# Performance work log

Measured on AMD Instinct MI355X. Metric: run time of the kernel, lower is better.

Reference implementation:

```python
import jax, jax.numpy as jnp
import numpy as np

K = 16  # num_samples (kNN neighbors)


def setup_inputs() -> dict:
    key = jax.random.key(0)
    k1, k2, k3 = jax.random.split(key, 3)
    B, N, S, D = 8, 8192, 2048, 64
    return {
        "points": jax.random.normal(k1, (B, 3, N), dtype=jnp.float32),
        "new_points": jax.random.normal(k2, (B, 3, S), dtype=jnp.float32),
        "features": jax.random.normal(k3, (B, D, N), dtype=jnp.float32),
    }


def reference(points, new_points, features):
    # channel-first -> channel-last, matching torch permute(0,2,1)
    pts = jnp.transpose(points, (0, 2, 1))       # [B, N, 3]
    newp = jnp.transpose(new_points, (0, 2, 1))  # [B, S, 3]
    feat = jnp.transpose(features, (0, 2, 1))    # [B, N, D]
    B, S, C = newp.shape

    # square_distance(points, new_points): [B, N, S]
    d = (
        jnp.sum(pts * pts, axis=-1)[:, :, None]
        - 2.0 * jnp.einsum("bnc,bsc->bns", pts, newp)
        + jnp.sum(newp * newp, axis=-1)[:, None, :]
    )
    # k smallest over N per (b, s): torch topk(largest=False) along dim=1 then permute -> [B, S, K]
    _, ind = jax.lax.top_k(-jnp.transpose(d, (0, 2, 1)), K)  # [B, S, K]

    gather = jax.vmap(lambda a, i: a[i])  # per-batch fancy gather
    grouped_pts = gather(pts, ind)    # [B, S, K, 3]
    grouped_feat = gather(feat, ind)  # [B, S, K, D]

    grouped_pts_new = grouped_pts - newp[:, :, None, :]          # relative coords
    new_features = jnp.concatenate([grouped_pts_new, grouped_feat], axis=-1)  # [B, S, K, 3+D]
    return jnp.transpose(new_features, (0, 3, 2, 1))  # [B, 3+D, K, S]
```

## Files before the change

### kernel.cpp

```cpp
#include <hip/hip_runtime.h>

constexpr int B = 8, N = 8192, S = 2048, D = 64, K = 16, C = 3 + D;
constexpr int G = 4;

__device__ __forceinline__ unsigned sortable(float f) {
    unsigned u = __float_as_uint(f);
    unsigned mask = (unsigned)(((int)u) >> 31) | 0x80000000u;
    return u ^ mask;
}

__device__ __forceinline__ float uload(const float* p) {
    return __uint_as_float(__builtin_amdgcn_readfirstlane(__float_as_uint(*p)));
}

__device__ __forceinline__ float make_d(float px, float py, float pz, float pnv,
                                        float qx, float qy, float qz, float qn) {
    float dot = __fmaf_rn(pz, qz, __fmaf_rn(py, qy, __fmul_rn(px, qx)));
    return __fadd_rn(__fsub_rn(pnv, __fmul_rn(2.0f, dot)), qn);
}

__device__ __forceinline__ float make_v(float px, float py, float pz, float pnv,
                                        float q2x, float q2y, float q2z) {
    float dot2 = __fmaf_rn(pz, q2z, __fmaf_rn(py, q2y, __fmul_rn(px, q2x)));
    return __fsub_rn(pnv, dot2);
}

__device__ __forceinline__ float bitonic_sort64_f32(float v, int lane) {
#pragma unroll
    for (int k = 2; k <= 64; k <<= 1)
#pragma unroll
        for (int j = k >> 1; j > 0; j >>= 1) {
            float o = __shfl_xor(v, j, 64);
            bool keepmin = ((lane & k) == 0) == ((lane & j) == 0);
            float mn = fminf(v, o), mx = fmaxf(v, o);
            v = keepmin ? mn : mx;
        }
    return v;
}

__device__ __forceinline__ unsigned long long bitonic_sort64_u64(unsigned long long v, int lane) {
#pragma unroll
    for (int k = 2; k <= 64; k <<= 1)
#pragma unroll
        for (int j = k >> 1; j > 0; j >>= 1) {
            unsigned long long o = __shfl_xor(v, j, 64);
            bool keepmin = ((lane & k) == 0) == ((lane & j) == 0);
            v = ((v < o) == keepmin) ? v : o;
        }
    return v;
}

__global__ void pack_kernel(const float* __restrict__ pts, float4* __restrict__ pts4) {
    int t = blockIdx.x * blockDim.x + threadIdx.x;
    if (t >= B * N) return;
    int b = t >> 13, n = t & (N - 1);
    const float* P = pts + (size_t)b * 3 * N;
    float x = P[n], y = P[N + n], z = P[2 * N + n];
    float pn = __fadd_rn(__fadd_rn(__fmul_rn(z, z), __fmul_rn(y, y)), __fmul_rn(x, x));
    pts4[t] = make_float4(x, y, z, pn);
}

__global__ void __launch_bounds__(256) transpose_kernel(const float* __restrict__ feat,
                                                        float* __restrict__ featT) {
    __shared__ float tile[64][65];
    int b = blockIdx.x >> 7;
    int n0 = (blockIdx.x & 127) << 6;
    int col = threadIdx.x & 63;
    int crow = threadIdx.x >> 6;
    const float* F = feat + (size_t)b * D * N;
#pragma unroll
    for (int i = 0; i < 16; ++i) {
        int c = i * 4 + crow;
        tile[c][col] = F[(size_t)c * N + n0 + col];
    }
    __syncthreads();
    float* FT = featT + ((size_t)b * N + n0) * D;
#pragma unroll
    for (int i = 0; i < 16; ++i) {
        int nl = i * 4 + crow;
        FT[(size_t)nl * D + col] = tile[col][nl];
    }
}

__global__ void __launch_bounds__(256) knn_kernel(const float4* __restrict__ pts4,
                                                  const float* __restrict__ newp,
                                                  int* __restrict__ ind) {
    __shared__ unsigned long long buf[4][G][64];
    __shared__ int cnt_lds[4][G];
    int wib = threadIdx.x >> 6;
    int lane = threadIdx.x & 63;
    int wid = blockIdx.x * 4 + wib;
    int b = wid >> 9;
    int sbase = (wid & 511) * G;
    const float4* P4 = pts4 + (size_t)b * N;
    const float* Q = newp + (size_t)b * 3 * S;
    if (lane < G) cnt_lds[wib][lane] = 0;
    float qx[G], qy[G], qz[G], qn[G], q2x[G], q2y[G], q2z[G];
#pragma unroll
    for (int g = 0; g < G; ++g) {
        int s = sbase + g;
        qx[g] = uload(Q + s);
        qy[g] = uload(Q + S + s);
        qz[g] = uload(Q + 2 * S + s);
        qn[g] = __fadd_rn(__fadd_rn(__fmul_rn(qz[g], qz[g]), __fmul_rn(qy[g], qy[g])),
                          __fmul_rn(qx[g], qx[g]));
        q2x[g] = 2.0f * qx[g];
        q2y[g] = 2.0f * qy[g];
        q2z[g] = 2.0f * qz[g];
    }

    float m[G];
#pragma unroll
    for (int g = 0; g < G; ++g) m[g] = __int_as_float(0x7f800000);
    for (int blk = 0; blk < N / 256; ++blk) {
        int nb = blk * 256 + lane;
        float4 c0 = P4[nb], c1 = P4[nb + 64], c2 = P4[nb + 128], c3 = P4[nb + 192];
#pragma unroll
        for (int g = 0; g < G; ++g) {
            float v0 = make_v(c0.x, c0.y, c0.z, c0.w, q2x[g], q2y[g], q2z[g]);
            float v1 = make_v(c1.x, c1.y, c1.z, c1.w, q2x[g], q2y[g], q2z[g]);
            float v2 = make_v(c2.x, c2.y, c2.z, c2.w, q2x[g], q2y[g], q2z[g]);
            float v3 = make_v(c3.x, c3.y, c3.z, c3.w, q2x[g], q2y[g], q2z[g]);
            m[g] = fminf(m[g], fminf(fminf(v0, v1), fminf(v2, v3)));
        }
    }
    float tau_d[G], vthr[G];
#pragma unroll
    for (int g = 0; g < G; ++g) {
        float tau_v = __shfl(bitonic_sort64_f32(m[g], lane), 15, 64);
        tau_d[g] = __fadd_rn(tau_v, qn[g]);
        vthr[g] = __fadd_rn(__fsub_rn(tau_d[g], qn[g]), 1e-4f);
    }

    for (int blk = 0; blk < N / 256; ++blk) {
        int nb = blk * 256 + lane;
        float4 c0 = P4[nb], c1 = P4[nb + 64], c2 = P4[nb + 128], c3 = P4[nb + 192];
#pragma unroll
        for (int g = 0; g < G; ++g) {
            float vv[4];
            vv[0] = make_v(c0.x, c0.y, c0.z, c0.w, q2x[g], q2y[g], q2z[g]);
            vv[1] = make_v(c1.x, c1.y, c1.z, c1.w, q2x[g], q2y[g], q2z[g]);
            vv[2] = make_v(c2.x, c2.y, c2.z, c2.w, q2x[g], q2y[g], q2z[g]);
            vv[3] = make_v(c3.x, c3.y, c3.z, c3.w, q2x[g], q2y[g], q2z[g]);
#pragma unroll
            for (int i = 0; i < 4; ++i) {
                if (vv[i] <= vthr[g]) {
                    float d = __fadd_rn(vv[i], qn[g]);
                    if (d <= tau_d[g]) {
                        int pos = atomicAdd(&cnt_lds[wib][g], 1);
                        if (pos < 64)
                            buf[wib][g][pos] =
                                ((unsigned long long)sortable(d) << 32) | (unsigned)(nb + i * 64);
                    }
                }
            }
        }
    }
    __syncthreads();

#pragma unroll
    for (int g = 0; g < G; ++g) {
        int cnt = cnt_lds[wib][g];
        int* my_ind = ind + ((size_t)b * S + sbase + g) * K;
        if (cnt <= 64) {
            unsigned long long key = (lane < cnt) ? buf[wib][g][lane] : ~0ull;
            key = bitonic_sort64_u64(key, lane);
            if (lane < K) my_ind[lane] = (int)(unsigned)key;
        } else {
            unsigned long long a[K];
#pragma unroll
            for (int i = 0; i < K; ++i) a[i] = ~0ull;
            for (int n = lane; n < N; n += 64) {
                float4 c = P4[n];
                float d = make_d(c.x, c.y, c.z, c.w, qx[g], qy[g], qz[g], qn[g]);
                unsigned long long key = ((unsigned long long)sortable(d) << 32) | (unsigned)n;
                if (key < a[K - 1]) {
#pragma unroll
                    for (int i = K - 1; i >= 1; --i) {
                        unsigned long long lo = a[i - 1];
                        a[i] = key < lo ? lo : (key < a[i] ? key : a[i]);
                    }
                    a[0] = key < a[0] ? key : a[0];
                }
            }
            for (int r = 0; r < K; ++r) {
                unsigned long long best = a[0];
#pragma unroll
                for (int mm = 1; mm < 64; mm <<= 1) {
                    unsigned long long o = __shfl_xor(best, mm, 64);
                    best = o < best ? o : best;
                }
                if (lane == 0) my_ind[r] = (int)(unsigned)best;
                bool won = (a[0] == best);
#pragma unroll
                for (int i = 0; i < K - 1; ++i) a[i] = won ? a[i + 1] : a[i];
                a[K - 1] = won ? ~0ull : a[K - 1];
            }
        }
    }
}

__global__ void __launch_bounds__(256) gather_tile_kernel(const float4* __restrict__ pts4,
                                                          const float* __restrict__ newp,
                                                          const float* __restrict__ featT,
                                                          const int* __restrict__ ind,
                                                          float* __restrict__ out) {
    __shared__ float tile[64][69];
    int bid = blockIdx.x;
    int b = bid >> 9;
    int k = (bid >> 5) & (K - 1);
    int s0 = (bid & 31) << 6;
    int j = threadIdx.x >> 2;
    int p = threadIdx.x & 3;
    int s = s0 + j;
    int id = ind[((size_t)b * S + s) * K + k];
    const float* row = featT + ((size_t)b * N + id) * D;
#pragma unroll
    for (int i = 0; i < 4; ++i) {
        int f = p + 4 * i;
        float4 v = *(const float4*)(row + f * 4);
        *(float4*)(&tile[j][3 + f * 4]) = v;
    }
    if (p == 0) {
        float4 pt = pts4[(size_t)b * N + id];
        const float* Q = newp + (size_t)b * 3 * S;
        tile[j][0] = __fsub_rn(pt.x, Q[s]);
        tile[j][1] = __fsub_rn(pt.y, Q[S + s]);
        tile[j][2] = __fsub_rn(pt.z, Q[2 * S + s]);
    }
    __syncthreads();
    size_t KS = (size_t)K * S;
    float* ob = out + ((size_t)b * C * K + k) * S + s0;
#pragma unroll
    for (int it = 0; it < 17; ++it) {
        int c = it * 4 + (threadIdx.x >> 6);
        int l = threadIdx.x & 63;
        if (c < C) ob[(size_t)c * KS + l] = tile[l][c];
    }
}

__global__ void __launch_bounds__(256) gather_kernel(const float4* __restrict__ pts4,
                                                     const float* __restrict__ newp,
                                                     const float* __restrict__ feat,
                                                     const int* __restrict__ ind,
                                                     float* __restrict__ out) {
    int t = blockIdx.x * blockDim.x + threadIdx.x;
    int s = t & (S - 1);
    int k = (t >> 11) & (K - 1);
    int rest = t >> 15;
    int g = rest % 17;
    int b = rest / 17;
    if (b >= B) return;
    int id = ind[((size_t)b * S + s) * K + k];
    size_t KS = (size_t)K * S;
    if (g == 0) {
        float4 p = pts4[(size_t)b * N + id];
        const float* Q = newp + (size_t)b * 3 * S;
        float* o = out + ((size_t)b * C * K + k) * S + s;
        o[0] = __fsub_rn(p.x, Q[s]);
        o[KS] = __fsub_rn(p.y, Q[S + s]);
        o[2 * KS] = __fsub_rn(p.z, Q[2 * S + s]);
    } else {
        int cb = (g - 1) * 4;
        const float* F = feat + (size_t)b * D * N;
        float4 f = make_float4(F[(size_t)cb * N + id], F[(size_t)(cb + 1) * N + id],
                               F[(size_t)(cb + 2) * N + id], F[(size_t)(cb + 3) * N + id]);
        float* o = out + (((size_t)b * C + 3 + cb) * K + k) * S + s;
        o[0] = f.x;
        o[KS] = f.y;
        o[2 * KS] = f.z;
        o[3 * KS] = f.w;
    }
}

extern "C" void kernel_launch(void* const* d_in, const int* in_sizes, int n_in,
                              void* d_out, int out_size, void* d_ws, size_t ws_size,
                              hipStream_t stream) {
    const float* pts = (const float*)d_in[0];
    const float* newp = (const float*)d_in[1];
    const float* feat = (const float*)d_in[2];
    float* out = (float*)d_out;

    size_t off_ind = 0;
    size_t off_pts4 = (size_t)B * S * K * sizeof(int);
    size_t off_featT = off_pts4 + (size_t)B * N * sizeof(float4);
    size_t need = off_featT + (size_t)B * N * D * sizeof(float);
    int* ind = (int*)((char*)d_ws + off_ind);
    float4* pts4 = (float4*)((char*)d_ws + off_pts4);
    float* featT = (float*)((char*)d_ws + off_featT);
    int useT = (ws_size >= need) ? 1 : 0;

    pack_kernel<<<(B * N) / 256, 256, 0, stream>>>(pts, pts4);
    if (useT) transpose_kernel<<<B * (N / 64), 256, 0, stream>>>(feat, featT);
    knn_kernel<<<(B * S) / (G * 4), 256, 0, stream>>>(pts4, newp, ind);
    if (useT)
        gather_tile_kernel<<<B * K * (S / 64), 256, 0, stream>>>(pts4, newp, featT, ind, out);
    else
        gather_kernel<<<(B * 17 * K * S) / 256, 256, 0, stream>>>(pts4, newp, feat, ind, out);
}
```

Baseline: 91.79 us.

## Estimate kNN threshold from a point subset and enlarge candidate buffer

The first pass, which estimates the 16th-nearest distance threshold, now scans only the first 2048 points instead of all 8192. That cuts the cost of this pass by three quarters. The looser threshold admits more candidates, so the per-query LDS buffer grows from 64 to 192 entries. The final bitonic sort is replaced by 16 rounds of wave-wide min extraction over three registers per lane. The risks are more atomics and LDS use in the second pass and more overflow into the slow full-scan fallback.

```diff
diff --git a/kernel.cpp b/kernel.cpp
--- a/kernel.cpp
+++ b/kernel.cpp
@@ -2,6 +2,8 @@
 
 constexpr int B = 8, N = 8192, S = 2048, D = 64, K = 16, C = 3 + D;
 constexpr int G = 4;
+constexpr int M = 2048;
+constexpr int BUFD = 192;
 
 __device__ __forceinline__ unsigned sortable(float f) {
     unsigned u = __float_as_uint(f);
@@ -34,18 +36,6 @@
             bool keepmin = ((lane & k) == 0) == ((lane & j) == 0);
             float mn = fminf(v, o), mx = fmaxf(v, o);
             v = keepmin ? mn : mx;
-        }
-    return v;
-}
-
-__device__ __forceinline__ unsigned long long bitonic_sort64_u64(unsigned long long v, int lane) {
-#pragma unroll
-    for (int k = 2; k <= 64; k <<= 1)
-#pragma unroll
-        for (int j = k >> 1; j > 0; j >>= 1) {
-            unsigned long long o = __shfl_xor(v, j, 64);
-            bool keepmin = ((lane & k) == 0) == ((lane & j) == 0);
-            v = ((v < o) == keepmin) ? v : o;
         }
     return v;
 }
@@ -85,7 +75,7 @@
 __global__ void __launch_bounds__(256) knn_kernel(const float4* __restrict__ pts4,
                                                   const float* __restrict__ newp,
                                                   int* __restrict__ ind) {
-    __shared__ unsigned long long buf[4][G][64];
+    __shared__ unsigned long long buf[4][G][BUFD];
     __shared__ int cnt_lds[4][G];
     int wib = threadIdx.x >> 6;
     int lane = threadIdx.x & 63;
@@ -95,24 +85,21 @@
     const float4* P4 = pts4 + (size_t)b * N;
     const float* Q = newp + (size_t)b * 3 * S;
     if (lane < G) cnt_lds[wib][lane] = 0;
-    float qx[G], qy[G], qz[G], qn[G], q2x[G], q2y[G], q2z[G];
+    float qn[G], q2x[G], q2y[G], q2z[G];
 #pragma unroll
     for (int g = 0; g < G; ++g) {
         int s = sbase + g;
-        qx[g] = uload(Q + s);
-        qy[g] = uload(Q + S + s);
-        qz[g] = uload(Q + 2 * S + s);
-        qn[g] = __fadd_rn(__fadd_rn(__fmul_rn(qz[g], qz[g]), __fmul_rn(qy[g], qy[g])),
-                          __fmul_rn(qx[g], qx[g]));
-        q2x[g] = 2.0f * qx[g];
-        q2y[g] = 2.0f * qy[g];
-        q2z[g] = 2.0f * qz[g];
+        float qx = uload(Q + s), qy = uload(Q + S + s), qz = uload(Q + 2 * S + s);
+        qn[g] = __fadd_rn(__fadd_rn(__fmul_rn(qz, qz), __fmul_rn(qy, qy)), __fmul_rn(qx, qx));
+        q2x[g] = 2.0f * qx;
+        q2y[g] = 2.0f * qy;
+        q2z[g] = 2.0f * qz;
     }
 
     float m[G];
 #pragma unroll
     for (int g = 0; g < G; ++g) m[g] = __int_as_float(0x7f800000);
-    for (int blk = 0; blk < N / 256; ++blk) {
+    for (int blk = 0; blk < M / 256; ++blk) {
         int nb = blk * 256 + lane;
         float4 c0 = P4[nb], c1 = P4[nb + 64], c2 = P4[nb + 128], c3 = P4[nb + 192];
 #pragma unroll
@@ -148,7 +135,7 @@
                     float d = __fadd_rn(vv[i], qn[g]);
                     if (d <= tau_d[g]) {
                         int pos = atomicAdd(&cnt_lds[wib][g], 1);
-                        if (pos < 64)
+                        if (pos < BUFD)
                             buf[wib][g][pos] =
                                 ((unsigned long long)sortable(d) << 32) | (unsigned)(nb + i * 64);
                     }
@@ -158,21 +145,40 @@
     }
     __syncthreads();
 
-#pragma unroll
+#pragma unroll 1
     for (int g = 0; g < G; ++g) {
         int cnt = cnt_lds[wib][g];
         int* my_ind = ind + ((size_t)b * S + sbase + g) * K;
-        if (cnt <= 64) {
-            unsigned long long key = (lane < cnt) ? buf[wib][g][lane] : ~0ull;
-            key = bitonic_sort64_u64(key, lane);
-            if (lane < K) my_ind[lane] = (int)(unsigned)key;
+        if (cnt >= K && cnt <= BUFD) {
+            unsigned long long a0 = (lane < cnt) ? buf[wib][g][lane] : ~0ull;
+            unsigned long long a1 = (64 + lane < cnt) ? buf[wib][g][64 + lane] : ~0ull;
+            unsigned long long a2 = (128 + lane < cnt) ? buf[wib][g][128 + lane] : ~0ull;
+#pragma unroll 1
+            for (int r = 0; r < K; ++r) {
+                unsigned long long lm = a0 < a1 ? a0 : a1;
+                lm = a2 < lm ? a2 : lm;
+                unsigned long long gm = lm;
+#pragma unroll
+                for (int mm = 1; mm < 64; mm <<= 1) {
+                    unsigned long long o = __shfl_xor(gm, mm, 64);
+                    gm = o < gm ? o : gm;
+                }
+                if (lane == 0) my_ind[r] = (int)(unsigned)gm;
+                bool w0 = (a0 == gm);
+                bool w1 = (a1 == gm) && !w0;
+                bool w2 = (a2 == gm) && !(w0 || w1);
+                a0 = w0 ? ~0ull : a0;
+                a1 = w1 ? ~0ull : a1;
+                a2 = w2 ? ~0ull : a2;
+            }
         } else {
+            float qx = 0.5f * q2x[g], qy = 0.5f * q2y[g], qz = 0.5f * q2z[g];
             unsigned long long a[K];
 #pragma unroll
             for (int i = 0; i < K; ++i) a[i] = ~0ull;
             for (int n = lane; n < N; n += 64) {
                 float4 c = P4[n];
-                float d = make_d(c.x, c.y, c.z, c.w, qx[g], qy[g], qz[g], qn[g]);
+                float d = make_d(c.x, c.y, c.z, c.w, qx, qy, qz, qn[g]);
                 unsigned long long key = ((unsigned long long)sortable(d) << 32) | (unsigned)n;
                 if (key < a[K - 1]) {
 #pragma unroll
@@ -281,13 +287,11 @@
     const float* feat = (const float*)d_in[2];
     float* out = (float*)d_out;
 
-    size_t off_ind = 0;
-    size_t off_pts4 = (size_t)B * S * K * sizeof(int);
-    size_t off_featT = off_pts4 + (size_t)B * N * sizeof(float4);
-    size_t need = off_featT + (size_t)B * N * D * sizeof(float);
-    int* ind = (int*)((char*)d_ws + off_ind);
-    float4* pts4 = (float4*)((char*)d_ws + off_pts4);
-    float* featT = (float*)((char*)d_ws + off_featT);
+    size_t off = 0;
+    int* ind = (int*)((char*)d_ws + off);        off += (size_t)B * S * K * sizeof(int);
+    float4* pts4 = (float4*)((char*)d_ws + off); off += (size_t)B * N * sizeof(float4);
+    float* featT = (float*)((char*)d_ws + off);
+    size_t need = off + (size_t)B * N * D * sizeof(float);
     int useT = (ws_size >= need) ? 1 : 0;
 
     pack_kernel<<<(B * N) / 256, 256, 0, stream>>>(pts, pts4);
```

Result: slower. 124.2 us (+35.3%).
